# Optimization experiments

Hardware: AMD Instinct MI355X
Metric: run time of the kernel (lower is better)

The kernel has to match this reference:

```python
import jax, jax.numpy as jnp
import numpy as np
import math

N = 4096
D = 256
H = 8
DH = D // H
E_RAND = 131072
EPS = 1e-5


def _layernorm(x, g, b):
    mu = jnp.mean(x, axis=-1, keepdims=True)
    var = jnp.mean((x - mu) ** 2, axis=-1, keepdims=True)
    return (x - mu) * jax.lax.rsqrt(var + EPS) * g + b


def setup_inputs() -> dict:
    key = jax.random.key(0)
    ks = jax.random.split(key, 16)
    s = 1.0 / math.sqrt(D)
    x = jax.random.normal(ks[0], (N, D), dtype=jnp.float32)
    src = jax.random.randint(ks[1], (E_RAND,), 0, N)
    dst = jax.random.randint(ks[2], (E_RAND,), 0, N)
    loop = jnp.arange(N)
    edge_index = jnp.stack([jnp.concatenate([src, loop]),
                            jnp.concatenate([dst, loop])]).astype(jnp.int64)
    def lin(k):
        return jax.random.normal(k, (D, D), dtype=jnp.float32) * s
    return {
        "x": x,
        "edge_index": edge_index,
        "Wq": lin(ks[3]), "bq": jnp.zeros((D,), jnp.float32),
        "Wk": lin(ks[4]), "bk": jnp.zeros((D,), jnp.float32),
        "Wv": lin(ks[5]), "bv": jnp.zeros((D,), jnp.float32),
        "Wo": lin(ks[6]), "bo": jnp.zeros((D,), jnp.float32),
        "g1": jnp.ones((D,), jnp.float32), "b1": jnp.zeros((D,), jnp.float32),
        "g2": jnp.ones((D,), jnp.float32), "b2": jnp.zeros((D,), jnp.float32),
        "Wm1": jax.random.normal(ks[7], (D, 2 * D), jnp.float32) * s,
        "bm1": jnp.zeros((2 * D,), jnp.float32),
        "Wm2": jax.random.normal(ks[8], (2 * D, D), jnp.float32) * (1.0 / math.sqrt(2 * D)),
        "bm2": jnp.zeros((D,), jnp.float32),
    }


def reference(x, edge_index, Wq, bq, Wk, bk, Wv, bv, Wo, bo,
              g1, b1, g2, b2, Wm1, bm1, Wm2, bm2):
    scale = 1.0 / math.sqrt(DH)
    h = _layernorm(x, g1, b1)
    # [N, D] -> [H, N, DH]
    q = (h @ Wq + bq).reshape(N, H, DH).transpose(1, 0, 2)
    k = (h @ Wk + bk).reshape(N, H, DH).transpose(1, 0, 2)
    v = (h @ Wv + bv).reshape(N, H, DH).transpose(1, 0, 2)
    att = jnp.einsum('hnd,hmd->hnm', q, k) * scale  # [H, N, N]
    # mask: True everywhere except edges (edge positions are attended)
    mask = jnp.ones((N, N), dtype=bool).at[edge_index[0], edge_index[1]].set(False)
    att = jnp.where(mask[None, :, :], -jnp.inf, att)
    att = jax.nn.softmax(att, axis=-1)
    y = jnp.einsum('hnm,hmd->hnd', att, v)  # [H, N, DH]
    y = y.transpose(1, 0, 2).reshape(N, D)
    x = x + (y @ Wo + bo)
    h2 = _layernorm(x, g2, b2)
    x = x + (jax.nn.gelu(h2 @ Wm1 + bm1, approximate=False) @ Wm2 + bm2)
    return x
```

## Files before the change

### kernel.cpp

```cpp
#include <hip/hip_runtime.h>
#include <hip/hip_bf16.h>

#define N_NODES 4096
#define D_MODEL 256
#define NWORDS 128
#define CAP 96

typedef __attribute__((ext_vector_type(8))) short short8;
typedef __attribute__((ext_vector_type(4))) short short4v;
typedef __attribute__((ext_vector_type(4))) float f32x4;

__device__ __forceinline__ unsigned short f2b(float f) {
    unsigned u = __float_as_uint(f);
    return (unsigned short)((u + 0x7FFFu + ((u >> 16) & 1u)) >> 16);
}
__device__ __forceinline__ float b2f(unsigned short u) {
    return __uint_as_float((unsigned)u << 16);
}
__device__ __forceinline__ unsigned pk2(float lo, float hi) {
    unsigned r;
    asm("v_cvt_pk_bf16_f32 %0, %1, %2" : "=v"(r) : "v"(lo), "v"(hi));
    return r;
}
__device__ __forceinline__ uint4 scale8(short8 v, float p) {
    uint4 r;
    r.x = pk2(b2f((unsigned short)v[0]) * p, b2f((unsigned short)v[1]) * p);
    r.y = pk2(b2f((unsigned short)v[2]) * p, b2f((unsigned short)v[3]) * p);
    r.z = pk2(b2f((unsigned short)v[4]) * p, b2f((unsigned short)v[5]) * p);
    r.w = pk2(b2f((unsigned short)v[6]) * p, b2f((unsigned short)v[7]) * p);
    return r;
}

__global__ __launch_bounds__(256) void prep_kernel(const float* __restrict__ Wq,
        const float* __restrict__ Wk, const float* __restrict__ Wv,
        const float* __restrict__ Wo, const float* __restrict__ Wm1,
        const float* __restrict__ Wm2, unsigned short* __restrict__ wbf,
        uint4* __restrict__ bitmap, const int* __restrict__ ei,
        int* __restrict__ flag, const float* __restrict__ x,
        const float* __restrict__ g1, const float* __restrict__ b1,
        unsigned short* __restrict__ h) {
    int b = blockIdx.x, t = threadIdx.x;
    if (b < 128) {
        const float* W; int base, K, M, kt, mt;
        if (b < 64)      { int r = b >> 4; W = (r == 0) ? Wq : (r == 1) ? Wk : (r == 2) ? Wv : Wo;
                           base = r << 16; K = 256; M = 256; kt = (b & 15) >> 2; mt = b & 3; }
        else if (b < 96) { W = Wm1; base = 262144; K = 256; M = 512; kt = (b - 64) >> 3; mt = (b - 64) & 7; }
        else             { W = Wm2; base = 393216; K = 512; M = 256; kt = (b - 96) >> 2; mt = (b - 96) & 3; }
        __shared__ unsigned short Lt[64][66];
        #pragma unroll
        for (int i = 0; i < 4; ++i) {
            int lin = i * 256 + t;
            int r = lin >> 4, c4 = (lin & 15) << 2;
            float4 v = *(const float4*)&W[(size_t)(kt * 64 + r) * M + mt * 64 + c4];
            Lt[r][c4 + 0] = f2b(v.x); Lt[r][c4 + 1] = f2b(v.y);
            Lt[r][c4 + 2] = f2b(v.z); Lt[r][c4 + 3] = f2b(v.w);
        }
        __syncthreads();
        #pragma unroll
        for (int i = 0; i < 2; ++i) {
            int lin = i * 256 + t;
            int mr = lin >> 3, kc = (lin & 7) << 3;
            short8 o;
            #pragma unroll
            for (int e = 0; e < 8; ++e) o[e] = (short)Lt[kc + e][mr];
            *(short8*)&wbf[base + (size_t)(mt * 64 + mr) * K + kt * 64 + kc] = o;
        }
    } else if (b < 640) {
        bitmap[(size_t)(b - 128) * 256 + t] = uint4{0, 0, 0, 0};
    } else if (b == 640) {
        if (t == 0) {
            int is64 = 1;
            for (int i = 1; i < 128; i += 2)
                if (ei[i] != 0) { is64 = 0; break; }
            *flag = is64;
        }
    } else {
        int row = b - 641;
        float v = x[row * D_MODEL + t];
        __shared__ float red[4];
        float s = v;
        #pragma unroll
        for (int off = 32; off; off >>= 1) s += __shfl_down(s, off, 64);
        if ((t & 63) == 0) red[t >> 6] = s;
        __syncthreads();
        float mu = (red[0] + red[1] + red[2] + red[3]) * (1.0f / 256.0f);
        __syncthreads();
        float d = v - mu;
        float s2 = d * d;
        #pragma unroll
        for (int off = 32; off; off >>= 1) s2 += __shfl_down(s2, off, 64);
        if ((t & 63) == 0) red[t >> 6] = s2;
        __syncthreads();
        float var = (red[0] + red[1] + red[2] + red[3]) * (1.0f / 256.0f);
        h[row * D_MODEL + t] = f2b(d * rsqrtf(var + 1e-5f) * g1[t] + b1[t]);
    }
}

template <int K, int BM, int MODE, bool LNA, bool STATS>
__global__ __launch_bounds__(512) void gemm_bf16(const unsigned short* __restrict__ A,
        const float* __restrict__ Af, const float* __restrict__ psum,
        const float* __restrict__ psum2, const float* __restrict__ lng,
        const float* __restrict__ lnb, const unsigned short* __restrict__ BT,
        const float* __restrict__ bias, const float* __restrict__ bias_k,
        const float* __restrict__ bias_v, const float* __restrict__ R,
        float* __restrict__ Cf, unsigned short* __restrict__ Cb,
        unsigned short* __restrict__ Ck, unsigned short* __restrict__ Cv,
        float* __restrict__ opsum, float* __restrict__ opsum2, int M,
        const int* __restrict__ ei, int E, const int* __restrict__ flag,
        unsigned* __restrict__ bitmap, int nadj) {
    constexpr int MR = BM / 64;
    constexpr int NRB = 4096 / BM;
    int tid = threadIdx.x;
    if (MODE == 3 && (int)blockIdx.x < nadj) {
        int e = (int)blockIdx.x * 512 + tid;
        if (e < E) {
            int n, m;
            if (*flag) { n = ei[2 * e]; m = ei[2 * (E + e)]; }
            else       { n = ei[e];     m = ei[E + e]; }
            atomicOr(&bitmap[n * NWORDS + (m >> 5)], 1u << (m & 31));
        }
        return;
    }
    __shared__ unsigned short Asm[BM][72];
    __shared__ unsigned short Bsm[64][72];
    __shared__ float psA[64][2], psA2[64][2];
    __shared__ float muS[BM], invS[BM];

    int bx2  = (MODE == 3) ? ((int)blockIdx.x - nadj) : 0;
    int brow = (MODE == 3) ? ((bx2 % NRB) * BM) : ((int)blockIdx.x * BM);
    int by   = (MODE == 3) ? (bx2 / NRB) : (int)blockIdx.y;
    int bcol = by << 6;
    int wid = tid >> 6, lane = tid & 63;
    int wr = wid >> 1, wc = wid & 1;
    int l15 = lane & 15, lhi = lane >> 4;
    int r0 = tid >> 3, c0 = (tid & 7) << 3;

    float mu_r[MR], inv_r[MR];
    if (LNA) {
        if (tid < BM) {
            float4 s4 = ((const float4*)psum)[brow + tid];
            float4 q4 = ((const float4*)psum2)[brow + tid];
            float S  = s4.x + s4.y + s4.z + s4.w;
            float S2 = q4.x + q4.y + q4.z + q4.w;
            float mu = S * (1.0f / 256.0f);
            muS[tid] = mu;
            invS[tid] = rsqrtf(S2 * (1.0f / 256.0f) - mu * mu + 1e-5f);
        }
        __syncthreads();
        #pragma unroll
        for (int m = 0; m < MR; ++m) { mu_r[m] = muS[r0 + m * 64]; inv_r[m] = invS[r0 + m * 64]; }
    }

    const unsigned short* Bp = BT + (size_t)(bcol + r0) * K + c0;
    f32x4 acc[MR][2] = {};
    short8 areg[MR];
    float4 xa[MR], xb[MR], ga, gb, ba, bb;
    if (LNA) {
        #pragma unroll
        for (int m = 0; m < MR; ++m) {
            const float* Xp = Af + (size_t)(brow + r0 + m * 64) * 256 + c0;
            xa[m] = *(const float4*)(Xp);
            xb[m] = *(const float4*)(Xp + 4);
        }
        ga = *(const float4*)(lng + c0); gb = *(const float4*)(lng + c0 + 4);
        ba = *(const float4*)(lnb + c0); bb = *(const float4*)(lnb + c0 + 4);
    } else {
        #pragma unroll
        for (int m = 0; m < MR; ++m)
            areg[m] = *(const short8*)(A + (size_t)(brow + r0 + m * 64) * K + c0);
    }
    short8 breg = *(const short8*)(Bp);

    #pragma unroll
    for (int k0 = 0; k0 < K; k0 += 64) {
        if (LNA) {
            #pragma unroll
            for (int m = 0; m < MR; ++m) {
                float xv[8] = {xa[m].x, xa[m].y, xa[m].z, xa[m].w,
                               xb[m].x, xb[m].y, xb[m].z, xb[m].w};
                float gv[8] = {ga.x, ga.y, ga.z, ga.w, gb.x, gb.y, gb.z, gb.w};
                float bv[8] = {ba.x, ba.y, ba.z, ba.w, bb.x, bb.y, bb.z, bb.w};
                short8 o;
                #pragma unroll
                for (int j = 0; j < 8; ++j)
                    o[j] = (short)f2b((xv[j] - mu_r[m]) * inv_r[m] * gv[j] + bv[j]);
                *(short8*)&Asm[r0 + m * 64][c0] = o;
            }
        } else {
            #pragma unroll
            for (int m = 0; m < MR; ++m)
                *(short8*)&Asm[r0 + m * 64][c0] = areg[m];
        }
        *(short8*)&Bsm[r0][c0] = breg;
        __syncthreads();
        if (k0 + 64 < K) {
            if (LNA) {
                #pragma unroll
                for (int m = 0; m < MR; ++m) {
                    const float* Xp = Af + (size_t)(brow + r0 + m * 64) * 256 + k0 + 64 + c0;
                    xa[m] = *(const float4*)(Xp);
                    xb[m] = *(const float4*)(Xp + 4);
                }
                ga = *(const float4*)(lng + k0 + 64 + c0);
                gb = *(const float4*)(lng + k0 + 64 + c0 + 4);
                ba = *(const float4*)(lnb + k0 + 64 + c0);
                bb = *(const float4*)(lnb + k0 + 64 + c0 + 4);
            } else {
                #pragma unroll
                for (int m = 0; m < MR; ++m)
                    areg[m] = *(const short8*)(A + (size_t)(brow + r0 + m * 64) * K + k0 + 64 + c0);
            }
            breg = *(const short8*)(Bp + k0 + 64);
        }
        #pragma unroll
        for (int ks = 0; ks < 2; ++ks) {
            int kc = ks * 32 + lhi * 8;
            short8 b_0 = *(const short8*)&Bsm[wc * 32 + l15][kc];
            short8 b_1 = *(const short8*)&Bsm[wc * 32 + 16 + l15][kc];
            #pragma unroll
            for (int sm = 0; sm < MR; ++sm) {
                short8 a_s = *(const short8*)&Asm[wr * 16 * MR + sm * 16 + l15][kc];
                acc[sm][0] = __builtin_amdgcn_mfma_f32_16x16x32_bf16(a_s, b_0, acc[sm][0], 0, 0, 0);
                acc[sm][1] = __builtin_amdgcn_mfma_f32_16x16x32_bf16(a_s, b_1, acc[sm][1], 0, 0, 0);
            }
        }
        __syncthreads();
    }

    float cs[2][4];
    #pragma unroll
    for (int sm = 0; sm < MR; ++sm)
        #pragma unroll
        for (int sn = 0; sn < 2; ++sn) {
            int col = bcol + wc * 32 + sn * 16 + l15;
            float bs;
            if (MODE == 3)
                bs = (col < 256) ? bias[col]
                   : (col < 512) ? bias_k[col - 256] : bias_v[col - 512];
            else
                bs = bias[col];
            #pragma unroll
            for (int r = 0; r < 4; ++r) {
                int row = brow + wr * 16 * MR + sm * 16 + lhi * 4 + r;
                float c = acc[sm][sn][r] + bs;
                if (MODE == 1) {
                    c = 0.5f * c * (1.0f + erff(c * 0.70710678118654752f));
                    Cb[(size_t)row * M + col] = f2b(c);
                } else if (MODE == 2) {
                    c += R[(size_t)row * M + col];
                    Cf[(size_t)row * M + col] = c;
                } else if (MODE == 3) {
                    int part = col >> 8, cc = col & 255;
                    unsigned short* dst = (part == 0) ? Cb : (part == 1) ? Ck : Cv;
                    dst[(((size_t)(cc >> 5) * N_NODES + row) << 5) + (cc & 31)] = f2b(c);
                } else {
                    Cb[(size_t)row * M + col] = f2b(c);
                }
                if (STATS) cs[sn][r] = c;
            }
        }
    if (STATS) {
        #pragma unroll
        for (int r = 0; r < 4; ++r) {
            float s  = cs[0][r] + cs[1][r];
            float s2 = cs[0][r] * cs[0][r] + cs[1][r] * cs[1][r];
            #pragma unroll
            for (int off = 1; off < 16; off <<= 1) {
                s  += __shfl_xor(s, off, 64);
                s2 += __shfl_xor(s2, off, 64);
            }
            if (l15 == 0) {
                int rl = wr * 16 + lhi * 4 + r;
                psA[rl][wc] = s; psA2[rl][wc] = s2;
            }
        }
        __syncthreads();
        if (tid < 64) {
            opsum [(size_t)(brow + tid) * 4 + by] = psA[tid][0] + psA[tid][1];
            opsum2[(size_t)(brow + tid) * 4 + by] = psA2[tid][0] + psA2[tid][1];
        }
    }
}

#define TRLOAD(dst_, OFF_) \
    asm volatile("ds_read_b64_tr_b16 %0, %1 offset:" #OFF_ \
                 : "=v"(dst_) : "v"(trbase))
#define PVSUM(tv_) { \
    acc0 += b2f((unsigned short)tv_[0]); acc1 += b2f((unsigned short)tv_[1]); \
    acc0 += b2f((unsigned short)tv_[2]); acc1 += b2f((unsigned short)tv_[3]); }

__global__ __launch_bounds__(256) void attn_kernel(const unsigned short* __restrict__ qh,
        const unsigned short* __restrict__ kh, const unsigned short* __restrict__ vh,
        const unsigned* __restrict__ bitmap, unsigned short* __restrict__ y) {
    int bid = blockIdx.x, tid = threadIdx.x;
    int h = bid & 7, oct = bid >> 3;
    int g = tid >> 5, lane = tid & 31;
    int n = oct * 8 + g;
    __shared__ int sIdx[8][CAP];
    __shared__ unsigned short Vst[8][2176];

    const unsigned short* qp = qh + (((size_t)h * N_NODES + n) << 5);
    float qreg[32];
    #pragma unroll
    for (int i = 0; i < 4; ++i) {
        short8 q8 = *(const short8*)(qp + i * 8);
        #pragma unroll
        for (int j = 0; j < 8; ++j) qreg[i * 8 + j] = b2f((unsigned short)q8[j]);
    }

    uint4 w4 = ((const uint4*)(bitmap + (size_t)n * NWORDS))[lane];
    unsigned words[4] = {w4.x, w4.y, w4.z, w4.w};
    int pc = __popc(w4.x) + __popc(w4.y) + __popc(w4.z) + __popc(w4.w);
    int pre = pc;
    #pragma unroll
    for (int off = 1; off < 32; off <<= 1) {
        int u = __shfl_up(pre, off, 32);
        if (lane >= off) pre += u;
    }
    int c = __shfl(pre, 31, 32);
    int off = pre - pc;
    #pragma unroll
    for (int i = 0; i < 4; ++i) {
        unsigned word = words[i];
        int wbase = ((lane << 2) + i) << 5;
        while (word) {
            int bit = __ffs(word) - 1;
            word &= word - 1;
            if (off < CAP) sIdx[g][off] = wbase + bit;
            ++off;
        }
    }
    c = min(c, CAP);
    for (int i = c + lane; i < 64; i += 32) sIdx[g][i] = 0;
    __syncthreads();

    int idx_a = sIdx[g][lane], idx_b = sIdx[g][lane + 32];
    const size_t hb = (size_t)h * N_NODES << 5;

    const unsigned short* va = vh + hb + ((size_t)idx_a << 5);
    const unsigned short* vb = vh + hb + ((size_t)idx_b << 5);
    short8 va0 = *(const short8*)(va);      short8 va1 = *(const short8*)(va + 8);
    short8 va2 = *(const short8*)(va + 16); short8 va3 = *(const short8*)(va + 24);
    short8 vb0 = *(const short8*)(vb);      short8 vb1 = *(const short8*)(vb + 8);
    short8 vb2 = *(const short8*)(vb + 16); short8 vb3 = *(const short8*)(vb + 24);

    const unsigned short* ka = kh + hb + ((size_t)idx_a << 5);
    const unsigned short* kb = kh + hb + ((size_t)idx_b << 5);
    short8 ka0 = *(const short8*)(ka);      short8 ka1 = *(const short8*)(ka + 8);
    short8 ka2 = *(const short8*)(ka + 16); short8 ka3 = *(const short8*)(ka + 24);
    short8 kb0 = *(const short8*)(kb);      short8 kb1 = *(const short8*)(kb + 8);
    short8 kb2 = *(const short8*)(kb + 16); short8 kb3 = *(const short8*)(kb + 24);

    float da0 = 0.f, da1 = 0.f, db0 = 0.f, db1 = 0.f;
    #pragma unroll
    for (int e = 0; e < 8; ++e) {
        da0 = fmaf(qreg[e],      b2f((unsigned short)ka0[e]), da0);
        da1 = fmaf(qreg[8 + e],  b2f((unsigned short)ka1[e]), da1);
        da0 = fmaf(qreg[16 + e], b2f((unsigned short)ka2[e]), da0);
        da1 = fmaf(qreg[24 + e], b2f((unsigned short)ka3[e]), da1);
        db0 = fmaf(qreg[e],      b2f((unsigned short)kb0[e]), db0);
        db1 = fmaf(qreg[8 + e],  b2f((unsigned short)kb1[e]), db1);
        db0 = fmaf(qreg[16 + e], b2f((unsigned short)kb2[e]), db0);
        db1 = fmaf(qreg[24 + e], b2f((unsigned short)kb3[e]), db1);
    }
    const float sc = 0.17677669529663687f;
    float s_a = (lane < c)      ? (da0 + da1) * sc : -INFINITY;
    float s_b = (lane + 32 < c) ? (db0 + db1) * sc : -INFINITY;

    float bm = fmaxf(s_a, s_b);
    #pragma unroll
    for (int o2 = 16; o2; o2 >>= 1) bm = fmaxf(bm, __shfl_xor(bm, o2, 32));
    float p_a = (lane < c)      ? __expf(s_a - bm) : 0.0f;
    float p_b = (lane + 32 < c) ? __expf(s_b - bm) : 0.0f;
    float S = p_a + p_b;
    #pragma unroll
    for (int o2 = 16; o2; o2 >>= 1) S += __shfl_xor(S, o2, 32);

    {
        unsigned short* vr = &Vst[g][(lane >> 2) * 136 + (lane & 3) * 16];
        *(uint4*)(vr + 0)  = scale8(va0, p_a);
        *(uint4*)(vr + 8)  = scale8(va1, p_a);
        *(uint4*)(vr + 64) = scale8(va2, p_a);
        *(uint4*)(vr + 72) = scale8(va3, p_a);
        unsigned short* vr2 = vr + 8 * 136;
        *(uint4*)(vr2 + 0)  = scale8(vb0, p_b);
        *(uint4*)(vr2 + 8)  = scale8(vb1, p_b);
        *(uint4*)(vr2 + 64) = scale8(vb2, p_b);
        *(uint4*)(vr2 + 72) = scale8(vb3, p_b);
    }

    unsigned trbase = (unsigned)(uintptr_t)(&Vst[g][0])
                    + ((unsigned)(lane >> 4) << 7) + ((unsigned)(lane & 15) << 3);
    asm volatile("s_waitcnt lgkmcnt(0)" ::: "memory");
    short4v t0, t1, t2, t3, t4, t5, t6, t7, t8, t9, t10, t11, t12, t13, t14, t15;
    TRLOAD(t0, 0);     TRLOAD(t1, 272);  TRLOAD(t2, 544);  TRLOAD(t3, 816);
    TRLOAD(t4, 1088);  TRLOAD(t5, 1360); TRLOAD(t6, 1632); TRLOAD(t7, 1904);
    TRLOAD(t8, 2176);  TRLOAD(t9, 2448); TRLOAD(t10, 2720); TRLOAD(t11, 2992);
    TRLOAD(t12, 3264); TRLOAD(t13, 3536); TRLOAD(t14, 3808); TRLOAD(t15, 4080);
    asm volatile("s_waitcnt lgkmcnt(0)" ::: "memory");
    __builtin_amdgcn_sched_barrier(0);

    float acc0 = 0.0f, acc1 = 0.0f;
    PVSUM(t0)  PVSUM(t1)  PVSUM(t2)  PVSUM(t3)
    PVSUM(t4)  PVSUM(t5)  PVSUM(t6)  PVSUM(t7)
    PVSUM(t8)  PVSUM(t9)  PVSUM(t10) PVSUM(t11)
    PVSUM(t12) PVSUM(t13) PVSUM(t14) PVSUM(t15)
    float acc = acc0 + acc1;

    if (c > 64) {
        float m_run = bm;
        for (int b0 = 64; b0 < c; b0 += 32) {
            int j = b0 + lane;
            float s = -INFINITY;
            if (j < c) {
                const unsigned short* kp = kh + hb + ((size_t)sIdx[g][j] << 5);
                float d = 0.0f;
                #pragma unroll
                for (int i = 0; i < 4; ++i) {
                    short8 k8 = *(const short8*)(kp + i * 8);
                    #pragma unroll
                    for (int e = 0; e < 8; ++e)
                        d = fmaf(qreg[i * 8 + e], b2f((unsigned short)k8[e]), d);
                }
                s = d * sc;
            }
            float bm2 = s;
            #pragma unroll
            for (int o2 = 16; o2; o2 >>= 1) bm2 = fmaxf(bm2, __shfl_xor(bm2, o2, 32));
            float newM = fmaxf(m_run, bm2);
            float p = (j < c) ? __expf(s - newM) : 0.0f;
            float bs = p;
            #pragma unroll
            for (int o2 = 16; o2; o2 >>= 1) bs += __shfl_xor(bs, o2, 32);
            float scale = __expf(m_run - newM);
            S = S * scale + bs;
            acc *= scale;
            int lim = min(32, c - b0);
            const unsigned short* vbase = vh + hb + lane;
            for (int jj = 0; jj < lim; ++jj) {
                float pj = __shfl(p, jj, 32);
                acc = fmaf(pj, b2f(vbase[(size_t)sIdx[g][b0 + jj] << 5]), acc);
            }
            m_run = newM;
        }
    }
    y[(size_t)n * 256 + h * 32 + lane] = f2b(acc / S);
}

extern "C" void kernel_launch(void* const* d_in, const int* in_sizes, int n_in,
                              void* d_out, int out_size, void* d_ws, size_t ws_size,
                              hipStream_t stream) {
    const float* x   = (const float*)d_in[0];
    const int*   ei  = (const int*)d_in[1];
    const float* Wq  = (const float*)d_in[2];  const float* bq  = (const float*)d_in[3];
    const float* Wk  = (const float*)d_in[4];  const float* bk  = (const float*)d_in[5];
    const float* Wv  = (const float*)d_in[6];  const float* bv  = (const float*)d_in[7];
    const float* Wo  = (const float*)d_in[8];  const float* bo  = (const float*)d_in[9];
    const float* g1  = (const float*)d_in[10]; const float* b1  = (const float*)d_in[11];
    const float* g2  = (const float*)d_in[12]; const float* b2  = (const float*)d_in[13];
    const float* Wm1 = (const float*)d_in[14]; const float* bm1 = (const float*)d_in[15];
    const float* Wm2 = (const float*)d_in[16]; const float* bm2 = (const float*)d_in[17];
    float* out = (float*)d_out;
    int E = in_sizes[1] / 2;
    int nadj = (E + 511) / 512;

    char* WS = (char*)d_ws;
    const size_t MB = 1u << 20;
    unsigned*       bitmap = (unsigned*)WS;
    int*            flag   = (int*)(WS + 2 * MB);
    float*          psum   = (float*)(WS + 2 * MB + 4096);
    float*          psum2  = (float*)(WS + 2 * MB + 4096 + 65536);
    unsigned short* wbf    = (unsigned short*)(WS + 3 * MB);
    unsigned short* y      = (unsigned short*)(WS + 4 * MB);
    float*          x1     = (float*)(WS + 6 * MB);
    unsigned short* m1     = (unsigned short*)(WS + 10 * MB);
    unsigned short* h      = (unsigned short*)(WS + 14 * MB);
    unsigned short* qh     = (unsigned short*)(WS + 16 * MB);
    unsigned short* kh     = (unsigned short*)(WS + 18 * MB);
    unsigned short* vh     = (unsigned short*)(WS + 20 * MB);

    const unsigned short* WTqkv = wbf;
    const unsigned short* WTo   = wbf + 196608;
    const unsigned short* WTm1  = wbf + 262144;
    const unsigned short* WTm2  = wbf + 393216;

    prep_kernel<<<4737, 256, 0, stream>>>(Wq, Wk, Wv, Wo, Wm1, Wm2, wbf,
                                          (uint4*)bitmap, ei, flag, x, g1, b1, h);
    gemm_bf16<256, 128, 3, false, false><<<nadj + 384, 512, 0, stream>>>(h, nullptr,
            nullptr, nullptr, nullptr, nullptr, WTqkv, bq, bk, bv, nullptr,
            nullptr, qh, kh, vh, nullptr, nullptr, 768, ei, E, flag, bitmap, nadj);
    attn_kernel<<<N_NODES, 256, 0, stream>>>(qh, kh, vh, bitmap, y);
    gemm_bf16<256, 64, 2, false, true><<<dim3(64, 4), 512, 0, stream>>>(y, nullptr,
            nullptr, nullptr, nullptr, nullptr, WTo, bo, nullptr, nullptr, x,
            x1, nullptr, nullptr, nullptr, psum, psum2, 256, nullptr, 0, nullptr, nullptr, 0);
    gemm_bf16<256, 128, 1, true, false><<<dim3(32, 8), 512, 0, stream>>>(nullptr, x1,
            psum, psum2, g2, b2, WTm1, bm1, nullptr, nullptr, nullptr,
            nullptr, m1, nullptr, nullptr, nullptr, nullptr, 512, nullptr, 0, nullptr, nullptr, 0);
    gemm_bf16<512, 64, 2, false, false><<<dim3(64, 4), 512, 0, stream>>>(m1, nullptr,
            nullptr, nullptr, nullptr, nullptr, WTm2, bm2, nullptr, nullptr, x1,
            out, nullptr, nullptr, nullptr, nullptr, nullptr, 256, nullptr, 0, nullptr, nullptr, 0);
}
```

Before: 71.47 us.

## Map one 64-lane wavefront per attention row and shrink GEMM row tiles

The attention kernel now gives each destination node a full 64-lane wavefront instead of a 32-lane half, so each lane handles one neighbor. The overflow path now processes 64 neighbors per step with the same LDS transpose-read PV reduction instead of a serial per-neighbor loop. Two half-row partial sums are combined with a cross-lane shuffle, and the grid doubles to 8192 blocks. The block-level __syncthreads is dropped, each wave working only on its own shared-memory slice. Separately, the QKV and MLP1 GEMMs use 64-row tiles with twice as many blocks to raise parallelism, at the cost of more weight reloads.

```diff
diff --git a/kernel.cpp b/kernel.cpp
--- a/kernel.cpp
+++ b/kernel.cpp
@@ -4,7 +4,7 @@
 #define N_NODES 4096
 #define D_MODEL 256
 #define NWORDS 128
-#define CAP 96
+#define CAP 128
 
 typedef __attribute__((ext_vector_type(8))) short short8;
 typedef __attribute__((ext_vector_type(4))) short short4v;
@@ -293,11 +293,11 @@
         const unsigned short* __restrict__ kh, const unsigned short* __restrict__ vh,
         const unsigned* __restrict__ bitmap, unsigned short* __restrict__ y) {
     int bid = blockIdx.x, tid = threadIdx.x;
-    int h = bid & 7, oct = bid >> 3;
-    int g = tid >> 5, lane = tid & 31;
-    int n = oct * 8 + g;
-    __shared__ int sIdx[8][CAP];
-    __shared__ unsigned short Vst[8][2176];
+    int h = bid & 7;
+    int wid = tid >> 6, lane = tid & 63;
+    int n = ((bid >> 3) << 2) + wid;
+    __shared__ int sIdx[4][CAP];
+    __shared__ unsigned short Vst[4][2176];
 
     const unsigned short* qp = qh + (((size_t)h * N_NODES + n) << 5);
     float qreg[32];
@@ -308,143 +308,143 @@
         for (int j = 0; j < 8; ++j) qreg[i * 8 + j] = b2f((unsigned short)q8[j]);
     }
 
-    uint4 w4 = ((const uint4*)(bitmap + (size_t)n * NWORDS))[lane];
-    unsigned words[4] = {w4.x, w4.y, w4.z, w4.w};
-    int pc = __popc(w4.x) + __popc(w4.y) + __popc(w4.z) + __popc(w4.w);
+    uint2 w2 = ((const uint2*)(bitmap + (size_t)n * NWORDS))[lane];
+    unsigned words[2] = {w2.x, w2.y};
+    int pc = __popc(w2.x) + __popc(w2.y);
     int pre = pc;
     #pragma unroll
-    for (int off = 1; off < 32; off <<= 1) {
-        int u = __shfl_up(pre, off, 32);
+    for (int off = 1; off < 64; off <<= 1) {
+        int u = __shfl_up(pre, off, 64);
         if (lane >= off) pre += u;
     }
-    int c = __shfl(pre, 31, 32);
+    int c = __shfl(pre, 63, 64);
     int off = pre - pc;
     #pragma unroll
-    for (int i = 0; i < 4; ++i) {
+    for (int i = 0; i < 2; ++i) {
         unsigned word = words[i];
-        int wbase = ((lane << 2) + i) << 5;
+        int wbase = ((lane << 1) + i) << 5;
         while (word) {
             int bit = __ffs(word) - 1;
             word &= word - 1;
-            if (off < CAP) sIdx[g][off] = wbase + bit;
+            if (off < CAP) sIdx[wid][off] = wbase + bit;
             ++off;
         }
     }
     c = min(c, CAP);
-    for (int i = c + lane; i < 64; i += 32) sIdx[g][i] = 0;
-    __syncthreads();
-
-    int idx_a = sIdx[g][lane], idx_b = sIdx[g][lane + 32];
+    for (int i = c + lane; i < CAP; i += 64) sIdx[wid][i] = 0;
+
+    int idx = sIdx[wid][lane];
     const size_t hb = (size_t)h * N_NODES << 5;
 
-    const unsigned short* va = vh + hb + ((size_t)idx_a << 5);
-    const unsigned short* vb = vh + hb + ((size_t)idx_b << 5);
-    short8 va0 = *(const short8*)(va);      short8 va1 = *(const short8*)(va + 8);
-    short8 va2 = *(const short8*)(va + 16); short8 va3 = *(const short8*)(va + 24);
-    short8 vb0 = *(const short8*)(vb);      short8 vb1 = *(const short8*)(vb + 8);
-    short8 vb2 = *(const short8*)(vb + 16); short8 vb3 = *(const short8*)(vb + 24);
-
-    const unsigned short* ka = kh + hb + ((size_t)idx_a << 5);
-    const unsigned short* kb = kh + hb + ((size_t)idx_b << 5);
-    short8 ka0 = *(const short8*)(ka);      short8 ka1 = *(const short8*)(ka + 8);
-    short8 ka2 = *(const short8*)(ka + 16); short8 ka3 = *(const short8*)(ka + 24);
-    short8 kb0 = *(const short8*)(kb);      short8 kb1 = *(const short8*)(kb + 8);
-    short8 kb2 = *(const short8*)(kb + 16); short8 kb3 = *(const short8*)(kb + 24);
-
-    float da0 = 0.f, da1 = 0.f, db0 = 0.f, db1 = 0.f;
+    const unsigned short* va = vh + hb + ((size_t)idx << 5);
+    short8 v0 = *(const short8*)(va);      short8 v1 = *(const short8*)(va + 8);
+    short8 v2 = *(const short8*)(va + 16); short8 v3 = *(const short8*)(va + 24);
+    const unsigned short* ka = kh + hb + ((size_t)idx << 5);
+    short8 k0 = *(const short8*)(ka);      short8 k1 = *(const short8*)(ka + 8);
+    short8 k2 = *(const short8*)(ka + 16); short8 k3 = *(const short8*)(ka + 24);
+
+    float d0 = 0.f, d1 = 0.f, d2 = 0.f, d3 = 0.f;
     #pragma unroll
     for (int e = 0; e < 8; ++e) {
-        da0 = fmaf(qreg[e],      b2f((unsigned short)ka0[e]), da0);
-        da1 = fmaf(qreg[8 + e],  b2f((unsigned short)ka1[e]), da1);
-        da0 = fmaf(qreg[16 + e], b2f((unsigned short)ka2[e]), da0);
-        da1 = fmaf(qreg[24 + e], b2f((unsigned short)ka3[e]), da1);
-        db0 = fmaf(qreg[e],      b2f((unsigned short)kb0[e]), db0);
-        db1 = fmaf(qreg[8 + e],  b2f((unsigned short)kb1[e]), db1);
-        db0 = fmaf(qreg[16 + e], b2f((unsigned short)kb2[e]), db0);
-        db1 = fmaf(qreg[24 + e], b2f((unsigned short)kb3[e]), db1);
+        d0 = fmaf(qreg[e],      b2f((unsigned short)k0[e]), d0);
+        d1 = fmaf(qreg[8 + e],  b2f((unsigned short)k1[e]), d1);
+        d2 = fmaf(qreg[16 + e], b2f((unsigned short)k2[e]), d2);
+        d3 = fmaf(qreg[24 + e], b2f((unsigned short)k3[e]), d3);
     }
     const float sc = 0.17677669529663687f;
-    float s_a = (lane < c)      ? (da0 + da1) * sc : -INFINITY;
-    float s_b = (lane + 32 < c) ? (db0 + db1) * sc : -INFINITY;
-
-    float bm = fmaxf(s_a, s_b);
-    #pragma unroll
-    for (int o2 = 16; o2; o2 >>= 1) bm = fmaxf(bm, __shfl_xor(bm, o2, 32));
-    float p_a = (lane < c)      ? __expf(s_a - bm) : 0.0f;
-    float p_b = (lane + 32 < c) ? __expf(s_b - bm) : 0.0f;
-    float S = p_a + p_b;
-    #pragma unroll
-    for (int o2 = 16; o2; o2 >>= 1) S += __shfl_xor(S, o2, 32);
+    float s = (lane < c) ? ((d0 + d1) + (d2 + d3)) * sc : -INFINITY;
+
+    float bm = s;
+    #pragma unroll
+    for (int o2 = 32; o2; o2 >>= 1) bm = fmaxf(bm, __shfl_xor(bm, o2, 64));
+    float p = (lane < c) ? __expf(s - bm) : 0.0f;
+    float S = p;
+    #pragma unroll
+    for (int o2 = 32; o2; o2 >>= 1) S += __shfl_xor(S, o2, 64);
 
     {
-        unsigned short* vr = &Vst[g][(lane >> 2) * 136 + (lane & 3) * 16];
-        *(uint4*)(vr + 0)  = scale8(va0, p_a);
-        *(uint4*)(vr + 8)  = scale8(va1, p_a);
-        *(uint4*)(vr + 64) = scale8(va2, p_a);
-        *(uint4*)(vr + 72) = scale8(va3, p_a);
-        unsigned short* vr2 = vr + 8 * 136;
-        *(uint4*)(vr2 + 0)  = scale8(vb0, p_b);
-        *(uint4*)(vr2 + 8)  = scale8(vb1, p_b);
-        *(uint4*)(vr2 + 64) = scale8(vb2, p_b);
-        *(uint4*)(vr2 + 72) = scale8(vb3, p_b);
-    }
-
-    unsigned trbase = (unsigned)(uintptr_t)(&Vst[g][0])
-                    + ((unsigned)(lane >> 4) << 7) + ((unsigned)(lane & 15) << 3);
+        unsigned short* vr = &Vst[wid][(lane >> 2) * 136 + (lane & 3) * 16];
+        *(uint4*)(vr + 0)  = scale8(v0, p);
+        *(uint4*)(vr + 8)  = scale8(v1, p);
+        *(uint4*)(vr + 64) = scale8(v2, p);
+        *(uint4*)(vr + 72) = scale8(v3, p);
+    }
+
+    unsigned trbase = (unsigned)(uintptr_t)(&Vst[wid][0])
+                    + ((unsigned)(lane >> 5) * 272u)
+                    + (((unsigned)(lane >> 4) & 1u) << 7) + ((unsigned)(lane & 15) << 3);
     asm volatile("s_waitcnt lgkmcnt(0)" ::: "memory");
-    short4v t0, t1, t2, t3, t4, t5, t6, t7, t8, t9, t10, t11, t12, t13, t14, t15;
-    TRLOAD(t0, 0);     TRLOAD(t1, 272);  TRLOAD(t2, 544);  TRLOAD(t3, 816);
-    TRLOAD(t4, 1088);  TRLOAD(t5, 1360); TRLOAD(t6, 1632); TRLOAD(t7, 1904);
-    TRLOAD(t8, 2176);  TRLOAD(t9, 2448); TRLOAD(t10, 2720); TRLOAD(t11, 2992);
-    TRLOAD(t12, 3264); TRLOAD(t13, 3536); TRLOAD(t14, 3808); TRLOAD(t15, 4080);
+    short4v t0, t1, t2, t3, t4, t5, t6, t7;
+    TRLOAD(t0, 0);    TRLOAD(t1, 544);  TRLOAD(t2, 1088); TRLOAD(t3, 1632);
+    TRLOAD(t4, 2176); TRLOAD(t5, 2720); TRLOAD(t6, 3264); TRLOAD(t7, 3808);
     asm volatile("s_waitcnt lgkmcnt(0)" ::: "memory");
     __builtin_amdgcn_sched_barrier(0);
 
     float acc0 = 0.0f, acc1 = 0.0f;
-    PVSUM(t0)  PVSUM(t1)  PVSUM(t2)  PVSUM(t3)
-    PVSUM(t4)  PVSUM(t5)  PVSUM(t6)  PVSUM(t7)
-    PVSUM(t8)  PVSUM(t9)  PVSUM(t10) PVSUM(t11)
-    PVSUM(t12) PVSUM(t13) PVSUM(t14) PVSUM(t15)
+    PVSUM(t0) PVSUM(t1) PVSUM(t2) PVSUM(t3)
+    PVSUM(t4) PVSUM(t5) PVSUM(t6) PVSUM(t7)
     float acc = acc0 + acc1;
 
     if (c > 64) {
         float m_run = bm;
-        for (int b0 = 64; b0 < c; b0 += 32) {
+        for (int b0 = 64; b0 < c; b0 += 64) {
             int j = b0 + lane;
-            float s = -INFINITY;
-            if (j < c) {
-                const unsigned short* kp = kh + hb + ((size_t)sIdx[g][j] << 5);
-                float d = 0.0f;
-                #pragma unroll
-                for (int i = 0; i < 4; ++i) {
-                    short8 k8 = *(const short8*)(kp + i * 8);
-                    #pragma unroll
-                    for (int e = 0; e < 8; ++e)
-                        d = fmaf(qreg[i * 8 + e], b2f((unsigned short)k8[e]), d);
-                }
-                s = d * sc;
-            }
-            float bm2 = s;
-            #pragma unroll
-            for (int o2 = 16; o2; o2 >>= 1) bm2 = fmaxf(bm2, __shfl_xor(bm2, o2, 32));
+            int idx2 = sIdx[wid][b0 + lane];
+            const unsigned short* va2 = vh + hb + ((size_t)idx2 << 5);
+            short8 u0 = *(const short8*)(va2);      short8 u1 = *(const short8*)(va2 + 8);
+            short8 u2 = *(const short8*)(va2 + 16); short8 u3 = *(const short8*)(va2 + 24);
+            const unsigned short* ka2 = kh + hb + ((size_t)idx2 << 5);
+            short8 e0 = *(const short8*)(ka2);      short8 e1 = *(const short8*)(ka2 + 8);
+            short8 e2 = *(const short8*)(ka2 + 16); short8 e3 = *(const short8*)(ka2 + 24);
+            float f0 = 0.f, f1 = 0.f, f2 = 0.f, f3 = 0.f;
+            #pragma unroll
+            for (int e = 0; e < 8; ++e) {
+                f0 = fmaf(qreg[e],      b2f((unsigned short)e0[e]), f0);
+                f1 = fmaf(qreg[8 + e],  b2f((unsigned short)e1[e]), f1);
+                f2 = fmaf(qreg[16 + e], b2f((unsigned short)e2[e]), f2);
+                f3 = fmaf(qreg[24 + e], b2f((unsigned short)e3[e]), f3);
+            }
+            float s2v = (j < c) ? ((f0 + f1) + (f2 + f3)) * sc : -INFINITY;
+            float bm2 = s2v;
+            #pragma unroll
+            for (int o2 = 32; o2; o2 >>= 1) bm2 = fmaxf(bm2, __shfl_xor(bm2, o2, 64));
             float newM = fmaxf(m_run, bm2);
-            float p = (j < c) ? __expf(s - newM) : 0.0f;
-            float bs = p;
-            #pragma unroll
-            for (int o2 = 16; o2; o2 >>= 1) bs += __shfl_xor(bs, o2, 32);
+            float p2 = (j < c) ? __expf(s2v - newM) : 0.0f;
+            float bs = p2;
+            #pragma unroll
+            for (int o2 = 32; o2; o2 >>= 1) bs += __shfl_xor(bs, o2, 64);
             float scale = __expf(m_run - newM);
             S = S * scale + bs;
             acc *= scale;
-            int lim = min(32, c - b0);
-            const unsigned short* vbase = vh + hb + lane;
-            for (int jj = 0; jj < lim; ++jj) {
-                float pj = __shfl(p, jj, 32);
-                acc = fmaf(pj, b2f(vbase[(size_t)sIdx[g][b0 + jj] << 5]), acc);
-            }
+            unsigned short* vr = &Vst[wid][(lane >> 2) * 136 + (lane & 3) * 16];
+            *(uint4*)(vr + 0)  = scale8(u0, p2);
+            *(uint4*)(vr + 8)  = scale8(u1, p2);
+            *(uint4*)(vr + 64) = scale8(u2, p2);
+            *(uint4*)(vr + 72) = scale8(u3, p2);
+            asm volatile("s_waitcnt lgkmcnt(0)" ::: "memory");
+            short4v r0, r1, r2, r3, r4, r5, r6, r7;
+            TRLOAD(r0, 0);    TRLOAD(r1, 544);  TRLOAD(r2, 1088); TRLOAD(r3, 1632);
+            TRLOAD(r4, 2176); TRLOAD(r5, 2720); TRLOAD(r6, 3264); TRLOAD(r7, 3808);
+            asm volatile("s_waitcnt lgkmcnt(0)" ::: "memory");
+            __builtin_amdgcn_sched_barrier(0);
+            float g0 = 0.f, g1v = 0.f;
+            {
+                float acc0b = 0.f, acc1b = 0.f;
+                #define PVSUM2(tv_) { \
+                    acc0b += b2f((unsigned short)tv_[0]); acc1b += b2f((unsigned short)tv_[1]); \
+                    acc0b += b2f((unsigned short)tv_[2]); acc1b += b2f((unsigned short)tv_[3]); }
+                PVSUM2(r0) PVSUM2(r1) PVSUM2(r2) PVSUM2(r3)
+                PVSUM2(r4) PVSUM2(r5) PVSUM2(r6) PVSUM2(r7)
+                g0 = acc0b; g1v = acc1b;
+            }
+            acc += g0 + g1v;
             m_run = newM;
         }
     }
-    y[(size_t)n * 256 + h * 32 + lane] = f2b(acc / S);
+
+    float tot = acc + __shfl_xor(acc, 32, 64);
+    if (lane < 32)
+        y[(size_t)n * 256 + h * 32 + lane] = f2b(tot / S);
 }
 
 extern "C" void kernel_launch(void* const* d_in, const int* in_sizes, int n_in,
@@ -486,14 +486,14 @@
 
     prep_kernel<<<4737, 256, 0, stream>>>(Wq, Wk, Wv, Wo, Wm1, Wm2, wbf,
                                           (uint4*)bitmap, ei, flag, x, g1, b1, h);
-    gemm_bf16<256, 128, 3, false, false><<<nadj + 384, 512, 0, stream>>>(h, nullptr,
+    gemm_bf16<256, 64, 3, false, false><<<nadj + 768, 512, 0, stream>>>(h, nullptr,
             nullptr, nullptr, nullptr, nullptr, WTqkv, bq, bk, bv, nullptr,
             nullptr, qh, kh, vh, nullptr, nullptr, 768, ei, E, flag, bitmap, nadj);
-    attn_kernel<<<N_NODES, 256, 0, stream>>>(qh, kh, vh, bitmap, y);
+    attn_kernel<<<8192, 256, 0, stream>>>(qh, kh, vh, bitmap, y);
     gemm_bf16<256, 64, 2, false, true><<<dim3(64, 4), 512, 0, stream>>>(y, nullptr,
             nullptr, nullptr, nullptr, nullptr, WTo, bo, nullptr, nullptr, x,
             x1, nullptr, nullptr, nullptr, psum, psum2, 256, nullptr, 0, nullptr, nullptr, 0);
-    gemm_bf16<256, 128, 1, true, false><<<dim3(32, 8), 512, 0, stream>>>(nullptr, x1,
+    gemm_bf16<256, 64, 1, true, false><<<dim3(64, 8), 512, 0, stream>>>(nullptr, x1,
             psum, psum2, g2, b2, WTm1, bm1, nullptr, nullptr, nullptr,
             nullptr, m1, nullptr, nullptr, nullptr, nullptr, 512, nullptr, 0, nullptr, nullptr, 0);
     gemm_bf16<512, 64, 2, false, false><<<dim3(64, 4), 512, 0, stream>>>(m1, nullptr,
```

After: 67.20 us. 6.0% less time.
